# Kernel tuning notes

Hardware: AMD Instinct MI355X
Metric: run time of the kernel (lower is better)

## Reference

```python
import jax, jax.numpy as jnp
import numpy as np

LAT, LONG = 16, 12
C_IN, C_MID = 128, 128
GROUPS = C_IN // 8          # conv groups and GroupNorm groups = 16
E = 200_000                 # number of projection entries (edges)
N = 4096                    # out_size (number of target messages)
PAD = LONG // 2
EPS = 1e-5


def setup_inputs() -> dict:
    key = jax.random.key(0)
    ks = jax.random.split(key, 8)
    x = jax.random.normal(ks[0], (E, C_IN), dtype=jnp.float32)
    proj_index = jax.random.randint(ks[1], (4, E), 0, N * LAT * LONG, dtype=jnp.int64 if jax.config.jax_enable_x64 else jnp.int32)
    proj_delta = jax.random.uniform(ks[2], (4, E), dtype=jnp.float32)
    proj_src_index = jax.random.randint(ks[3], (E,), 0, E, dtype=jnp.int64 if jax.config.jax_enable_x64 else jnp.int32)
    # grouped circular Conv1d: weight [out, in/groups, k] = [128, 2048/16, 12]
    fan_in = (C_IN * LAT // GROUPS) * LONG
    bound = 1.0 / np.sqrt(fan_in)
    conv_w = jax.random.uniform(ks[4], (C_MID, C_IN * LAT // GROUPS, LONG), dtype=jnp.float32, minval=-bound, maxval=bound)
    conv_b = jax.random.uniform(ks[5], (C_MID,), dtype=jnp.float32, minval=-bound, maxval=bound)
    gn_w = jnp.ones((C_MID,), dtype=jnp.float32)
    gn_b = jnp.zeros((C_MID,), dtype=jnp.float32)
    return {"x": x, "out_size": N, "proj_index": proj_index, "proj_delta": proj_delta,
            "proj_src_index": proj_src_index, "conv_w": conv_w, "conv_b": conv_b,
            "gn_w": gn_w, "gn_b": gn_b}


def reference(x, out_size, proj_index, proj_delta, proj_src_index, conv_w, conv_b, gn_w, gn_b):
    # ---- ProjectLatLongSphere: 4 weighted scatter-adds onto the sphere grid ----
    splat = x[proj_src_index]                              # [E, C]
    x_proj = jnp.zeros((out_size * LAT * LONG, C_IN), dtype=x.dtype)
    for i in range(4):                                      # fixed small unroll
        x_proj = x_proj.at[proj_index[i]].add(splat * proj_delta[i][:, None])
    # [N, lat*long, C] -> [N, C, lat*long] -> [N, C*lat, long]
    x_grid = x_proj.reshape(out_size, LAT * LONG, C_IN).transpose(0, 2, 1)
    x_grid = x_grid.reshape(out_size, C_IN * LAT, LONG)

    # ---- grouped circular Conv1d ----
    xp = jnp.concatenate([x_grid[..., -PAD:], x_grid, x_grid[..., :PAD]], axis=-1)  # [N, C*lat, long+2*pad]
    y = jax.lax.conv_general_dilated(
        xp, conv_w, window_strides=(1,), padding='VALID',
        dimension_numbers=('NCH', 'OIH', 'NCH'), feature_group_count=GROUPS)        # [N, C_MID, long+1]
    y = jax.nn.silu(y + conv_b[None, :, None])

    # ---- AvgPool1d(kernel=long) over first `long` positions ----
    y = jnp.mean(y[:, :, :LONG], axis=-1)                   # [N, C_MID]

    # ---- GroupNorm(num_groups=GROUPS) on [N, C_MID] ----
    g = y.reshape(out_size, GROUPS, C_MID // GROUPS)
    mu = jnp.mean(g, axis=-1, keepdims=True)
    var = jnp.var(g, axis=-1, keepdims=True)
    g = (g - mu) * jax.lax.rsqrt(var + EPS)
    return g.reshape(out_size, C_MID) * gn_w + gn_b
```

## Files before the change

kernel.cpp:

```cpp
#include <hip/hip_runtime.h>
#include <hip/hip_fp16.h>
#include <cstdint>

#define LATN 16
#define LONGN 12
#define PP 192
#define CIN 128
#define CMID 128
#define EPSV 1e-5f
#define SPLIT 4
#define CHB 32
#define TST 36
#define UMAXA 4

typedef float v2f __attribute__((ext_vector_type(2)));
typedef float f32x4 __attribute__((ext_vector_type(4)));
typedef _Float16 half8 __attribute__((ext_vector_type(8)));


__global__ void count2_kernel(const int* __restrict__ pidx, int* __restrict__ counts, int E) {
    int e = blockIdx.x * 256 + threadIdx.x;
    if (e >= E) return;
#pragma unroll
    for (int i = 0; i < 4; i++) {
        int v = pidx[i * E + e];
        atomicAdd(&counts[v], 1);
    }
}

__global__ void scan1_kernel(const int* __restrict__ cnt, int* __restrict__ startp,
                             int* __restrict__ bsum) {
    __shared__ int sd[1024];
    int t = threadIdx.x, b = blockIdx.x;
    int v = cnt[b * 1024 + t];
    sd[t] = v;
    __syncthreads();
    for (int off = 1; off < 1024; off <<= 1) {
        int x = (t >= off) ? sd[t - off] : 0;
        __syncthreads();
        sd[t] += x;
        __syncthreads();
    }
    startp[b * 1024 + t] = sd[t] - v;
    if (t == 1023) bsum[b] = sd[t];
}

__global__ void scan2_kernel(int* __restrict__ bsum, int* __restrict__ grand, int nb) {
    __shared__ int sd[1024];
    int t = threadIdx.x;
    int v = (t < nb) ? bsum[t] : 0;
    sd[t] = v;
    __syncthreads();
    for (int off = 1; off < 1024; off <<= 1) {
        int x = (t >= off) ? sd[t - off] : 0;
        __syncthreads();
        sd[t] += x;
        __syncthreads();
    }
    if (t < nb) bsum[t] = sd[t] - v;
    if (t == 1023) *grand = sd[1023];
}

__global__ void addback_kernel(int* __restrict__ startp, const int* __restrict__ bsum,
                               int* __restrict__ cur) {
    int v = blockIdx.x * 1024 + threadIdx.x;
    int s = startp[v] + bsum[blockIdx.x];
    startp[v] = s;
    cur[v] = s;
}

__global__ void record_kernel(const int* __restrict__ pidx, const int* __restrict__ src_idx,
                              const float* __restrict__ delta, int* __restrict__ cur,
                              uint2* __restrict__ rec, int E) {
    int e = blockIdx.x * 256 + threadIdx.x;
    if (e >= E) return;
    int src = src_idx[e];
#pragma unroll
    for (int i = 0; i < 4; i++) {
        int v = pidx[i * E + e];
        int p = v - (v / PP) * PP;
        int pos = atomicAdd(&cur[v], 1);
        rec[pos] = make_uint2((uint32_t)src | ((uint32_t)p << 18),
                              __float_as_uint(delta[i * E + e]));
    }
}

__global__ void wt2_kernel(const float* __restrict__ w, uint32_t* __restrict__ wt2) {
    int id = blockIdx.x * 256 + threadIdx.x;
    if (id >= CIN * 6 * CMID) return;
    int o = id & 127;
    int kp = (id >> 7) % 6;
    int i = id / (128 * 6);
    float a = w[(o * 128 + i) * 12 + 2 * kp];
    float b = w[(o * 128 + i) * 12 + 2 * kp + 1];
    __half2 h = __floats2half2_rn(a, b);
    wt2[id] = *reinterpret_cast<uint32_t*>(&h);
}


__global__ void wA_kernel(const float* __restrict__ w, _Float16* __restrict__ wA) {
    int id = blockIdx.x * 256 + threadIdx.x;
    if (id >= 16 * 6 * 48 * 64) return;
    int lane = id & 63;
    int rest = id >> 6;
    int s = rest % 48;
    int mt = (rest / 48) % 6;
    int g = rest / (48 * 6);
    int m = mt * 16 + (lane & 15);
    int o = m / 12;
    int t = m - o * 12;
    int og = g * 8 + o;
    _Float16 vals[8];
#pragma unroll
    for (int j = 0; j < 8; j++) {
        int kh = s * 32 + (lane >> 4) * 8 + j;
        int c = kh / PP;
        int p = kh - c * PP;
        int lat = p / LONGN;
        int ll = p - lat * LONGN;
        int k = (ll - t + 18) % 12;
        vals[j] = (_Float16)w[((og)*128 + c * 16 + lat) * 12 + k];
    }
    *(uint4*)(wA + (size_t)id * 8) = *(const uint4*)vals;
}


__global__ __launch_bounds__(256, 5) void scatter_kernel(
    const float* __restrict__ x, const uint2* __restrict__ rec,
    const int* __restrict__ start2, _Float16* __restrict__ grid) {
    __shared__ __align__(16) float tile[PP * TST];
    __shared__ int s2c[PP + 1];

    const int bid = blockIdx.x;
    const int n = bid >> 2;
    const int b = bid & 3;
    const int tid = threadIdx.x;

    {
        float4 zz = {0.f, 0.f, 0.f, 0.f};
        float4* t4 = (float4*)tile;
        for (int idx = tid; idx < PP * TST / 4; idx += 256) t4[idx] = zz;
        for (int idx = tid; idx < PP + 1; idx += 256) s2c[idx] = start2[n * PP + idx];
    }
    __syncthreads();

    {
        const int il = tid & 7;
        const int slot = tid >> 3;
        const int cbase = b * CHB + il * 4;
        const int e1 = s2c[slot * 6 + 6];
        for (int e = s2c[slot * 6]; e < e1; e += UMAXA) {
            uint2 rv[UMAXA];
            float4 xv[UMAXA];
#pragma unroll
            for (int u = 0; u < UMAXA; u++) {
                if (e + u < e1) rv[u] = rec[e + u];
            }
#pragma unroll
            for (int u = 0; u < UMAXA; u++) {
                if (e + u < e1) {
                    int src = (int)(rv[u].x & 0x3FFFFu);
                    xv[u] = *(const float4*)(x + (size_t)src * CIN + cbase);
                }
            }
#pragma unroll
            for (int u = 0; u < UMAXA; u++) {
                if (e + u < e1) {
                    float dl = __uint_as_float(rv[u].y);
                    int p = (int)(rv[u].x >> 18);
                    float* tp = tile + p * TST + (((il + (p & 7)) & 7) << 2);
                    float4 t = *(const float4*)tp;
                    t.x += xv[u].x * dl;
                    t.y += xv[u].y * dl;
                    t.z += xv[u].z * dl;
                    t.w += xv[u].w * dl;
                    *(float4*)tp = t;
                }
            }
        }
    }
    __syncthreads();

    {
        const int c = tid & 31;
        const int pc = tid >> 5;
        const int gch = b * CHB + c;
        _Float16* gdst = grid + ((size_t)n * CIN + gch) * PP;
        const int il = c >> 2;
        const int cm = c & 3;
#pragma unroll
        for (int j16 = 0; j16 < 3; j16++) {
            int pbase = pc * 24 + j16 * 8;
            _Float16 hh[8];
#pragma unroll
            for (int i = 0; i < 8; i++) {
                int p = pbase + i;
                hh[i] = (_Float16)tile[p * TST + ((((il + (p & 7)) & 7) << 2) + cm)];
            }
            *(uint4*)(gdst + pbase) = *(const uint4*)hh;
        }
    }
}


__global__ __launch_bounds__(256, 5) void gemm_kernel(
    const _Float16* __restrict__ grid, const _Float16* __restrict__ wA,
    const float* __restrict__ conv_b, const float* __restrict__ gn_w,
    const float* __restrict__ gn_b, float* __restrict__ out) {
    __shared__ float Clds[96 * 66];

    const int bid = blockIdx.x;
    const int g = bid & 15;
    const int ntile = bid >> 4;
    const int tid = threadIdx.x;
    const int lane = tid & 63;
    const int wv = tid >> 6;
    const int mh = wv & 1;
    const int nh = wv >> 1;

    const int nn = lane & 15;
    const int h = lane >> 4;

    const _Float16* a0 = wA + ((size_t)(g * 6 + mh * 3) * 48) * 512 + lane * 8;
    const _Float16* a1 = a0 + (size_t)48 * 512;
    const _Float16* a2 = a1 + (size_t)48 * 512;
    const _Float16* b0 = grid + ((size_t)(ntile * 64 + nh * 32 + nn) * CIN + g * 8) * PP + h * 8;
    const _Float16* b1 = b0 + (size_t)16 * CIN * PP;

    f32x4 acc00 = {0.f, 0.f, 0.f, 0.f}, acc01 = {0.f, 0.f, 0.f, 0.f};
    f32x4 acc10 = {0.f, 0.f, 0.f, 0.f}, acc11 = {0.f, 0.f, 0.f, 0.f};
    f32x4 acc20 = {0.f, 0.f, 0.f, 0.f}, acc21 = {0.f, 0.f, 0.f, 0.f};

    half8 cA0 = *(const half8*)(a0);
    half8 cA1 = *(const half8*)(a1);
    half8 cA2 = *(const half8*)(a2);
    half8 cB0 = *(const half8*)(b0);
    half8 cB1 = *(const half8*)(b1);

#pragma unroll 4
    for (int s = 0; s < 48; s++) {
        half8 nA0 = cA0, nA1 = cA1, nA2 = cA2, nB0 = cB0, nB1 = cB1;
        if (s + 1 < 48) {
            nA0 = *(const half8*)(a0 + (size_t)(s + 1) * 512);
            nA1 = *(const half8*)(a1 + (size_t)(s + 1) * 512);
            nA2 = *(const half8*)(a2 + (size_t)(s + 1) * 512);
            nB0 = *(const half8*)(b0 + (size_t)(s + 1) * 32);
            nB1 = *(const half8*)(b1 + (size_t)(s + 1) * 32);
        }
        acc00 = __builtin_amdgcn_mfma_f32_16x16x32_f16(cA0, cB0, acc00, 0, 0, 0);
        acc10 = __builtin_amdgcn_mfma_f32_16x16x32_f16(cA1, cB0, acc10, 0, 0, 0);
        acc20 = __builtin_amdgcn_mfma_f32_16x16x32_f16(cA2, cB0, acc20, 0, 0, 0);
        acc01 = __builtin_amdgcn_mfma_f32_16x16x32_f16(cA0, cB1, acc01, 0, 0, 0);
        acc11 = __builtin_amdgcn_mfma_f32_16x16x32_f16(cA1, cB1, acc11, 0, 0, 0);
        acc21 = __builtin_amdgcn_mfma_f32_16x16x32_f16(cA2, cB1, acc21, 0, 0, 0);
        cA0 = nA0; cA1 = nA1; cA2 = nA2; cB0 = nB0; cB1 = nB1;
    }

    {
        const int mbase = mh * 48 + h * 4;
        const int ncol = nh * 32 + nn;
#pragma unroll
        for (int j = 0; j < 4; j++) {
            Clds[(mbase + j) * 66 + ncol] = acc00[j];
            Clds[(mbase + j) * 66 + ncol + 16] = acc01[j];
            Clds[(mbase + 16 + j) * 66 + ncol] = acc10[j];
            Clds[(mbase + 16 + j) * 66 + ncol + 16] = acc11[j];
            Clds[(mbase + 32 + j) * 66 + ncol] = acc20[j];
            Clds[(mbase + 32 + j) * 66 + ncol + 16] = acc21[j];
        }
    }
    __syncthreads();

    {
        const int o = tid & 7;
        const int oc = g * 8 + o;
        const float bias = conv_b[oc];
        const float gw = gn_w[oc], gb = gn_b[oc];
#pragma unroll
        for (int pp = 0; pp < 2; pp++) {
            const int nl = (tid >> 3) + pp * 32;
            float sv = 0.f;
#pragma unroll
            for (int t = 0; t < 12; t++) {
                float z = Clds[(o * 12 + t) * 66 + nl] + bias;
                sv += z / (1.f + __expf(-z));
            }
            sv *= (1.f / 12.f);
            float s1 = sv, s2 = sv * sv;
#pragma unroll
            for (int m = 1; m < 8; m <<= 1) {
                s1 += __shfl_xor(s1, m);
                s2 += __shfl_xor(s2, m);
            }
            float mu = s1 * 0.125f;
            float var = fmaxf(s2 * 0.125f - mu * mu, 0.f);
            float inv = rsqrtf(var + EPSV);
            out[(size_t)(ntile * 64 + nl) * CMID + oc] = (sv - mu) * inv * gw + gb;
        }
    }
}


__global__ __launch_bounds__(256, 5) void fused_kernel(
    const float* __restrict__ x, const uint2* __restrict__ rec,
    const int* __restrict__ start2, const uint32_t* __restrict__ wt2,
    const float* __restrict__ conv_b, const float* __restrict__ gn_w,
    const float* __restrict__ gn_b, float* __restrict__ out) {
    __shared__ __align__(16) float tile[PP * TST];
    __shared__ int s2c[PP + 1];

    const int bid = blockIdx.x;
    const int n = bid >> 2;
    const int b = bid & 3;
    const int tid = threadIdx.x;

    {
        float4 zz = {0.f, 0.f, 0.f, 0.f};
        float4* t4 = (float4*)tile;
        for (int idx = tid; idx < PP * TST / 4; idx += 256) t4[idx] = zz;
        for (int idx = tid; idx < PP + 1; idx += 256) s2c[idx] = start2[n * PP + idx];
    }
    __syncthreads();

    {
        const int il = tid & 7;
        const int slot = tid >> 3;
        const int cbase = b * CHB + il * 4;
        const int e1 = s2c[slot * 6 + 6];
        float* tbase = tile + il * 4;
        for (int e = s2c[slot * 6]; e < e1; e += UMAXA) {
            uint2 rv[UMAXA];
            float4 xv[UMAXA];
#pragma unroll
            for (int u = 0; u < UMAXA; u++) {
                if (e + u < e1) rv[u] = rec[e + u];
            }
#pragma unroll
            for (int u = 0; u < UMAXA; u++) {
                if (e + u < e1) {
                    int src = (int)(rv[u].x & 0x3FFFFu);
                    xv[u] = *(const float4*)(x + (size_t)src * CIN + cbase);
                }
            }
#pragma unroll
            for (int u = 0; u < UMAXA; u++) {
                if (e + u < e1) {
                    float dl = __uint_as_float(rv[u].y);
                    int p = (int)(rv[u].x >> 18);
                    float* tp = tbase + p * TST;
                    float4 t = *(const float4*)tp;
                    t.x += xv[u].x * dl;
                    t.y += xv[u].y * dl;
                    t.z += xv[u].z * dl;
                    t.w += xv[u].w * dl;
                    *(float4*)tp = t;
                }
            }
        }
    }
    __syncthreads();

    const int o_local = tid & 31;
    const int q = tid >> 5;
    const int g_local = o_local >> 3;
    const int o = b * CHB + o_local;
    const int ch = g_local * 8 + q;

    v2f acc2[6];
#pragma unroll
    for (int u = 0; u < 6; u++) acc2[u] = (v2f)(0.f);

    const uint32_t* wcol = wt2 + (size_t)(q * LATN) * 6 * CMID + o;

#pragma unroll
    for (int lat = 0; lat < LATN; lat++) {
        float r[12];
#pragma unroll
        for (int j = 0; j < 12; j++)
            r[j] = tile[(lat * LONGN + j) * TST + ch];
        v2f rp[12];
#pragma unroll
        for (int j = 0; j < 12; j++) {
            rp[j].x = r[(j + 6) % 12];
            rp[j].y = r[(j + 7) % 12];
        }
        const uint32_t* wrow = wcol + (size_t)(lat * 6) * CMID;
#pragma unroll
        for (int kp = 0; kp < 6; kp++) {
            uint32_t wp = wrow[kp * CMID];
            __half2 h2 = *reinterpret_cast<__half2*>(&wp);
            float wlo = __half2float(h2.x);
            float whi = __half2float(h2.y);
            v2f wl2 = {wlo, wlo}, wh2 = {whi, whi};
#pragma unroll
            for (int u = 0; u < 6; u++) {
                acc2[u] += wl2 * rp[(2 * kp + 2 * u) % 12];
                acc2[u] += wh2 * rp[(2 * kp + 2 * u + 1) % 12];
            }
        }
    }
    __syncthreads();

    float* pbuf = tile;
#pragma unroll
    for (int u = 0; u < 6; u++) {
        pbuf[(q * 12 + 2 * u) * 32 + o_local] = acc2[u].x;
        pbuf[(q * 12 + 2 * u + 1) * 32 + o_local] = acc2[u].y;
    }
    __syncthreads();

    float* gbuf = tile + 8 * 12 * 32;
    float sv = 0.f;
    if (tid < 32) {
        float bias = conv_b[b * CHB + tid];
#pragma unroll
        for (int t = 0; t < 12; t++) {
            float z = bias;
#pragma unroll
            for (int qq = 0; qq < 8; qq++) z += pbuf[(qq * 12 + t) * 32 + tid];
            sv += z / (1.f + __expf(-z));
        }
        sv *= (1.f / 12.f);
        gbuf[tid] = sv;
    }
    __syncthreads();
    if (tid < 32) {
        int gb = tid & ~7;
        float mu = 0.f, m2 = 0.f;
#pragma unroll
        for (int j = 0; j < 8; j++) {
            float v = gbuf[gb + j];
            mu += v;
            m2 += v * v;
        }
        mu *= 0.125f;
        float var = m2 * 0.125f - mu * mu;
        var = fmaxf(var, 0.f);
        float inv = rsqrtf(var + EPSV);
        int oc = b * CHB + tid;
        out[(size_t)n * CMID + oc] = (sv - mu) * inv * gn_w[oc] + gn_b[oc];
    }
}

extern "C" void kernel_launch(void* const* d_in, const int* in_sizes, int n_in,
                              void* d_out, int out_size, void* d_ws, size_t ws_size,
                              hipStream_t stream) {
    const float* x = (const float*)d_in[0];
    const int* pidx = (const int*)d_in[2];
    const float* delta = (const float*)d_in[3];
    const int* src_idx = (const int*)d_in[4];
    const float* conv_w = (const float*)d_in[5];
    const float* conv_b = (const float*)d_in[6];
    const float* gn_w = (const float*)d_in[7];
    const float* gn_b = (const float*)d_in[8];
    float* out = (float*)d_out;

    int E = in_sizes[0] / CIN;
    int N = out_size / CMID;
    int ncells = N * PP;

    char* ws = (char*)d_ws;
    size_t off = 0;
    auto alloc = [&](size_t bytes) {
        size_t cur = off;
        off = (off + bytes + 255) & ~(size_t)255;
        return cur;
    };
    int* count2 = (int*)(ws + alloc((size_t)ncells * 4));
    int* start2 = (int*)(ws + alloc((size_t)(ncells + 1) * 4));
    int* bsum   = (int*)(ws + alloc((size_t)1024 * 4));
    uint2* rec  = (uint2*)(ws + alloc((size_t)4 * E * 8));
    uint32_t* wt2 = (uint32_t*)(ws + alloc((size_t)CIN * 6 * CMID * 4));
    size_t wA_off = alloc((size_t)16 * 6 * 48 * 64 * 8 * 2);
    size_t grid_off = alloc((size_t)N * CIN * PP * 2);
    _Float16* wA = (_Float16*)(ws + wA_off);
    _Float16* gridbuf = (_Float16*)(ws + grid_off);
    bool two_pass = (off <= ws_size);

    hipMemsetAsync(count2, 0, (size_t)ncells * 4, stream);

    int gE = (E + 255) / 256;
    int nb = ncells / 1024;
    count2_kernel<<<gE, 256, 0, stream>>>(pidx, count2, E);
    scan1_kernel<<<nb, 1024, 0, stream>>>(count2, start2, bsum);
    scan2_kernel<<<1, 1024, 0, stream>>>(bsum, start2 + ncells, nb);
    addback_kernel<<<nb, 1024, 0, stream>>>(start2, bsum, count2);
    record_kernel<<<gE, 256, 0, stream>>>(pidx, src_idx, delta, count2, rec, E);

    if (two_pass) {
        wA_kernel<<<(16 * 6 * 48 * 64 + 255) / 256, 256, 0, stream>>>(conv_w, wA);
        scatter_kernel<<<N * SPLIT, 256, 0, stream>>>(x, rec, start2, gridbuf);
        gemm_kernel<<<16 * 64, 256, 0, stream>>>(gridbuf, wA, conv_b, gn_w, gn_b, out);
    } else {
        wt2_kernel<<<(CIN * 6 * CMID + 255) / 256, 256, 0, stream>>>(conv_w, wt2);
        fused_kernel<<<N * SPLIT, 256, 0, stream>>>(x, rec, start2, wt2, conv_b, gn_w, gn_b, out);
    }
}
```

Measured before the change: 320.4 us.

## Bucket records per 6-cell slot with padded counts to drop tail guards

Changes the CSR bucketing from one bucket per grid cell to one bucket per 6-cell slot (32 per message), which shrinks the count/scan arrays. Each slot's count is rounded up to a multiple of 4. Padding entries are prefilled with null records that point to an extra dummy tile row, so the scatter loop can run without per-element bounds checks. This cuts scan work and branch overhead in the scatter loop. In exchange it adds a fill pass over the record buffer, spends wasted gathers on padding records, and concentrates more atomic contention on fewer counters.

```diff
diff --git a/kernel.cpp b/kernel.cpp
--- a/kernel.cpp
+++ b/kernel.cpp
@@ -12,19 +12,25 @@
 #define CHB 32
 #define TST 36
 #define UMAXA 4
+#define SPN 32
 
 typedef float v2f __attribute__((ext_vector_type(2)));
 typedef float f32x4 __attribute__((ext_vector_type(4)));
 typedef _Float16 half8 __attribute__((ext_vector_type(8)));
 
 
-__global__ void count2_kernel(const int* __restrict__ pidx, int* __restrict__ counts, int E) {
-    int e = blockIdx.x * 256 + threadIdx.x;
-    if (e >= E) return;
+__global__ void count2_kernel(const int* __restrict__ pidx, int* __restrict__ counts,
+                              uint2* __restrict__ rec, int E, int padtot, int nthreads) {
+    int gid = blockIdx.x * 256 + threadIdx.x;
+    uint2 nullrec = make_uint2((uint32_t)PP << 18, 0u);
+    for (int j = gid; j < padtot; j += nthreads) rec[j] = nullrec;
+    if (gid >= E) return;
 #pragma unroll
     for (int i = 0; i < 4; i++) {
-        int v = pidx[i * E + e];
-        atomicAdd(&counts[v], 1);
+        int v = pidx[i * E + gid];
+        int n = v / PP;
+        int p = v - n * PP;
+        atomicAdd(&counts[n * SPN + p / 6], 1);
     }
 }
 
@@ -32,7 +38,7 @@
                              int* __restrict__ bsum) {
     __shared__ int sd[1024];
     int t = threadIdx.x, b = blockIdx.x;
-    int v = cnt[b * 1024 + t];
+    int v = (cnt[b * 1024 + t] + 3) & ~3;
     sd[t] = v;
     __syncthreads();
     for (int off = 1; off < 1024; off <<= 1) {
@@ -78,8 +84,9 @@
 #pragma unroll
     for (int i = 0; i < 4; i++) {
         int v = pidx[i * E + e];
-        int p = v - (v / PP) * PP;
-        int pos = atomicAdd(&cur[v], 1);
+        int n = v / PP;
+        int p = v - n * PP;
+        int pos = atomicAdd(&cur[n * SPN + p / 6], 1);
         rec[pos] = make_uint2((uint32_t)src | ((uint32_t)p << 18),
                               __float_as_uint(delta[i * E + e]));
     }
@@ -128,8 +135,8 @@
 __global__ __launch_bounds__(256, 5) void scatter_kernel(
     const float* __restrict__ x, const uint2* __restrict__ rec,
     const int* __restrict__ start2, _Float16* __restrict__ grid) {
-    __shared__ __align__(16) float tile[PP * TST];
-    __shared__ int s2c[PP + 1];
+    __shared__ __align__(16) float tile[(PP + 1) * TST];
+    __shared__ int sst[SPN + 1];
 
     const int bid = blockIdx.x;
     const int n = bid >> 2;
@@ -139,8 +146,8 @@
     {
         float4 zz = {0.f, 0.f, 0.f, 0.f};
         float4* t4 = (float4*)tile;
-        for (int idx = tid; idx < PP * TST / 4; idx += 256) t4[idx] = zz;
-        for (int idx = tid; idx < PP + 1; idx += 256) s2c[idx] = start2[n * PP + idx];
+        for (int idx = tid; idx < (PP + 1) * TST / 4; idx += 256) t4[idx] = zz;
+        if (tid < SPN + 1) sst[tid] = start2[n * SPN + tid];
     }
     __syncthreads();
 
@@ -148,34 +155,29 @@
         const int il = tid & 7;
         const int slot = tid >> 3;
         const int cbase = b * CHB + il * 4;
-        const int e1 = s2c[slot * 6 + 6];
-        for (int e = s2c[slot * 6]; e < e1; e += UMAXA) {
+        const int e0 = sst[slot];
+        const int e1 = sst[slot + 1];
+        for (int e = e0; e < e1; e += UMAXA) {
             uint2 rv[UMAXA];
             float4 xv[UMAXA];
 #pragma unroll
+            for (int u = 0; u < UMAXA; u++) rv[u] = rec[e + u];
+#pragma unroll
             for (int u = 0; u < UMAXA; u++) {
-                if (e + u < e1) rv[u] = rec[e + u];
+                int src = (int)(rv[u].x & 0x3FFFFu);
+                xv[u] = *(const float4*)(x + (size_t)src * CIN + cbase);
             }
 #pragma unroll
             for (int u = 0; u < UMAXA; u++) {
-                if (e + u < e1) {
-                    int src = (int)(rv[u].x & 0x3FFFFu);
-                    xv[u] = *(const float4*)(x + (size_t)src * CIN + cbase);
-                }
-            }
-#pragma unroll
-            for (int u = 0; u < UMAXA; u++) {
-                if (e + u < e1) {
-                    float dl = __uint_as_float(rv[u].y);
-                    int p = (int)(rv[u].x >> 18);
-                    float* tp = tile + p * TST + (((il + (p & 7)) & 7) << 2);
-                    float4 t = *(const float4*)tp;
-                    t.x += xv[u].x * dl;
-                    t.y += xv[u].y * dl;
-                    t.z += xv[u].z * dl;
-                    t.w += xv[u].w * dl;
-                    *(float4*)tp = t;
-                }
+                float dl = __uint_as_float(rv[u].y);
+                int p = (int)(rv[u].x >> 18);
+                float* tp = tile + p * TST + (((il + (p & 7)) & 7) << 2);
+                float4 t = *(const float4*)tp;
+                t.x += xv[u].x * dl;
+                t.y += xv[u].y * dl;
+                t.z += xv[u].z * dl;
+                t.w += xv[u].w * dl;
+                *(float4*)tp = t;
             }
         }
     }
@@ -306,8 +308,8 @@
     const int* __restrict__ start2, const uint32_t* __restrict__ wt2,
     const float* __restrict__ conv_b, const float* __restrict__ gn_w,
     const float* __restrict__ gn_b, float* __restrict__ out) {
-    __shared__ __align__(16) float tile[PP * TST];
-    __shared__ int s2c[PP + 1];
+    __shared__ __align__(16) float tile[(PP + 1) * TST];
+    __shared__ int sst[SPN + 1];
 
     const int bid = blockIdx.x;
     const int n = bid >> 2;
@@ -317,8 +319,8 @@
     {
         float4 zz = {0.f, 0.f, 0.f, 0.f};
         float4* t4 = (float4*)tile;
-        for (int idx = tid; idx < PP * TST / 4; idx += 256) t4[idx] = zz;
-        for (int idx = tid; idx < PP + 1; idx += 256) s2c[idx] = start2[n * PP + idx];
+        for (int idx = tid; idx < (PP + 1) * TST / 4; idx += 256) t4[idx] = zz;
+        if (tid < SPN + 1) sst[tid] = start2[n * SPN + tid];
     }
     __syncthreads();
 
@@ -326,35 +328,30 @@
         const int il = tid & 7;
         const int slot = tid >> 3;
         const int cbase = b * CHB + il * 4;
-        const int e1 = s2c[slot * 6 + 6];
+        const int e0 = sst[slot];
+        const int e1 = sst[slot + 1];
         float* tbase = tile + il * 4;
-        for (int e = s2c[slot * 6]; e < e1; e += UMAXA) {
+        for (int e = e0; e < e1; e += UMAXA) {
             uint2 rv[UMAXA];
             float4 xv[UMAXA];
 #pragma unroll
+            for (int u = 0; u < UMAXA; u++) rv[u] = rec[e + u];
+#pragma unroll
             for (int u = 0; u < UMAXA; u++) {
-                if (e + u < e1) rv[u] = rec[e + u];
+                int src = (int)(rv[u].x & 0x3FFFFu);
+                xv[u] = *(const float4*)(x + (size_t)src * CIN + cbase);
             }
 #pragma unroll
             for (int u = 0; u < UMAXA; u++) {
-                if (e + u < e1) {
-                    int src = (int)(rv[u].x & 0x3FFFFu);
-                    xv[u] = *(const float4*)(x + (size_t)src * CIN + cbase);
-                }
-            }
-#pragma unroll
-            for (int u = 0; u < UMAXA; u++) {
-                if (e + u < e1) {
-                    float dl = __uint_as_float(rv[u].y);
-                    int p = (int)(rv[u].x >> 18);
-                    float* tp = tbase + p * TST;
-                    float4 t = *(const float4*)tp;
-                    t.x += xv[u].x * dl;
-                    t.y += xv[u].y * dl;
-                    t.z += xv[u].z * dl;
-                    t.w += xv[u].w * dl;
-                    *(float4*)tp = t;
-                }
+                float dl = __uint_as_float(rv[u].y);
+                int p = (int)(rv[u].x >> 18);
+                float* tp = tbase + p * TST;
+                float4 t = *(const float4*)tp;
+                t.x += xv[u].x * dl;
+                t.y += xv[u].y * dl;
+                t.z += xv[u].z * dl;
+                t.w += xv[u].w * dl;
+                *(float4*)tp = t;
             }
         }
     }
@@ -457,7 +454,8 @@
 
     int E = in_sizes[0] / CIN;
     int N = out_size / CMID;
-    int ncells = N * PP;
+    int nslots = N * SPN;
+    int padtot = 4 * E + nslots * 3;
 
     char* ws = (char*)d_ws;
     size_t off = 0;
@@ -466,10 +464,10 @@
         off = (off + bytes + 255) & ~(size_t)255;
         return cur;
     };
-    int* count2 = (int*)(ws + alloc((size_t)ncells * 4));
-    int* start2 = (int*)(ws + alloc((size_t)(ncells + 1) * 4));
+    int* count2 = (int*)(ws + alloc((size_t)nslots * 4));
+    int* start2 = (int*)(ws + alloc((size_t)(nslots + 1) * 4));
     int* bsum   = (int*)(ws + alloc((size_t)1024 * 4));
-    uint2* rec  = (uint2*)(ws + alloc((size_t)4 * E * 8));
+    uint2* rec  = (uint2*)(ws + alloc((size_t)padtot * 8));
     uint32_t* wt2 = (uint32_t*)(ws + alloc((size_t)CIN * 6 * CMID * 4));
     size_t wA_off = alloc((size_t)16 * 6 * 48 * 64 * 8 * 2);
     size_t grid_off = alloc((size_t)N * CIN * PP * 2);
@@ -477,13 +475,13 @@
     _Float16* gridbuf = (_Float16*)(ws + grid_off);
     bool two_pass = (off <= ws_size);
 
-    hipMemsetAsync(count2, 0, (size_t)ncells * 4, stream);
+    hipMemsetAsync(count2, 0, (size_t)nslots * 4, stream);
 
     int gE = (E + 255) / 256;
-    int nb = ncells / 1024;
-    count2_kernel<<<gE, 256, 0, stream>>>(pidx, count2, E);
+    int nb = nslots / 1024;
+    count2_kernel<<<gE, 256, 0, stream>>>(pidx, count2, rec, E, padtot, gE * 256);
     scan1_kernel<<<nb, 1024, 0, stream>>>(count2, start2, bsum);
-    scan2_kernel<<<1, 1024, 0, stream>>>(bsum, start2 + ncells, nb);
+    scan2_kernel<<<1, 1024, 0, stream>>>(bsum, start2 + nslots, nb);
     addback_kernel<<<nb, 1024, 0, stream>>>(start2, bsum, count2);
     record_kernel<<<gE, 256, 0, stream>>>(pidx, src_idx, delta, count2, rec, E);
 
```

Result: faster. 289.2 us (-9.7%).
